# Performance work log

Measured on AMD Instinct MI355X. Metric: run time of the kernel, lower is better.

Reference implementation:

```python
import jax, jax.numpy as jnp
import numpy as np

NUM_NODES = 256
IN_FEAT = 64
HIDDEN = 512
N_CLASSES = 2
BATCH = 256


def setup_inputs() -> dict:
    key = jax.random.key(0)
    ks = jax.random.split(key, 10)
    return {
        "z": jax.random.normal(ks[0], (BATCH, 1, NUM_NODES, NUM_NODES), dtype=jnp.float32),
        "node_emb": jax.random.normal(ks[1], (NUM_NODES, IN_FEAT), dtype=jnp.float32),
        "w1": jax.random.normal(ks[2], (IN_FEAT, HIDDEN), dtype=jnp.float32) * (1.0 / np.sqrt(IN_FEAT)),
        "b1": jnp.zeros((HIDDEN,), dtype=jnp.float32),
        "w2": jax.random.normal(ks[3], (HIDDEN, HIDDEN), dtype=jnp.float32) * (1.0 / np.sqrt(HIDDEN)),
        "b2": jnp.zeros((HIDDEN,), dtype=jnp.float32),
        "w3": jax.random.normal(ks[4], (HIDDEN, HIDDEN), dtype=jnp.float32) * (1.0 / np.sqrt(HIDDEN)),
        "b3": jnp.zeros((HIDDEN,), dtype=jnp.float32),
        "fcw": jax.random.normal(ks[5], (HIDDEN, N_CLASSES), dtype=jnp.float32) * (1.0 / np.sqrt(HIDDEN)),
        "fcb": jnp.zeros((N_CLASSES,), dtype=jnp.float32),
    }


def reference(z, node_emb, w1, b1, w2, b2, w3, b3, fcw, fcb):
    # z: (B, 1, N, N) latent interpreted as weighted adjacency
    z_sq = jnp.squeeze(z, axis=1)                         # (B, N, N)
    A = jax.nn.sigmoid(z_sq)
    A = (A + jnp.swapaxes(A, 1, 2)) * 0.5                  # symmetrize
    A_hat = A + jnp.eye(A.shape[-1], dtype=A.dtype)[None]  # add self loops
    D_hat = jnp.sum(A_hat, axis=2) + 1e-6                  # (B, N) degrees
    d_inv_sqrt = D_hat ** -0.5
    # norm_A = D^{-1/2} A_hat D^{-1/2} via row/col scaling (same math as diag bmm)
    norm_A = A_hat * d_inv_sqrt[:, :, None] * d_inv_sqrt[:, None, :]

    X = jnp.broadcast_to(node_emb[None], (z.shape[0],) + node_emb.shape)  # (B, N, F)
    H1 = jax.nn.relu(jnp.einsum('bij,bjh->bih', norm_A, X @ w1 + b1))
    H2 = jax.nn.relu(jnp.einsum('bij,bjh->bih', norm_A, H1 @ w2 + b2))
    H3 = jax.nn.relu(jnp.einsum('bij,bjh->bih', norm_A, H2 @ w3 + b3))
    graph_emb = jnp.mean(H3, axis=1)                       # (B, H)
    logits = graph_emb @ fcw + fcb                         # (B, n_classes)
    return logits
```

## Files before the change

### kernel.cpp

```cpp
#include <hip/hip_runtime.h>
#include <stdint.h>

#define B_ 256
#define N_ 256
#define F_ 64
#define H_ 512

typedef _Float16 f16;
typedef _Float16 f16x8 __attribute__((ext_vector_type(8)));
typedef _Float16 f16x4 __attribute__((ext_vector_type(4)));
typedef float    f32x4 __attribute__((ext_vector_type(4)));

__device__ __forceinline__ float sigmoidf_(float x) {
    return 1.0f / (1.0f + __expf(-x));
}

__global__ __launch_bounds__(256) void k_sums(const float* __restrict__ z,
                                              f16* __restrict__ S,
                                              float* __restrict__ R,
                                              float* __restrict__ Cpart) {
    int b = blockIdx.y, c = blockIdx.x;
    int tid = threadIdx.x, lane = tid & 63, w = tid >> 6;
    float colacc[4] = {0.f, 0.f, 0.f, 0.f};
    for (int r = 0; r < 16; r++) {
        int i = c * 64 + w * 16 + r;
        size_t base = ((size_t)(b * N_ + i)) * N_;
        float4 v = *(const float4*)(z + base + lane * 4);
        float s0 = sigmoidf_(v.x), s1 = sigmoidf_(v.y),
              s2 = sigmoidf_(v.z), s3 = sigmoidf_(v.w);
        f16x4 sv = { (f16)s0, (f16)s1, (f16)s2, (f16)s3 };
        *(f16x4*)(S + base + lane * 4) = sv;
        colacc[0] += s0; colacc[1] += s1; colacc[2] += s2; colacc[3] += s3;
        float rs = s0 + s1 + s2 + s3;
        for (int off = 32; off; off >>= 1) rs += __shfl_down(rs, off, 64);
        if (lane == 0) R[b * N_ + i] = rs;
    }
    __shared__ float cbuf[4][N_];
    #pragma unroll
    for (int k = 0; k < 4; k++) cbuf[w][lane * 4 + k] = colacc[k];
    __syncthreads();
    float s4 = cbuf[0][tid] + cbuf[1][tid] + cbuf[2][tid] + cbuf[3][tid];
    Cpart[((size_t)c * B_ + b) * N_ + tid] = s4;
}

__global__ __launch_bounds__(256) void k_norma3(const f16* __restrict__ S,
                                                const float* __restrict__ R,
                                                const float* __restrict__ Cpart,
                                                f16* __restrict__ nA) {
    __shared__ f16 T0[128 * 129];
    __shared__ f16 T1[128 * 129];
    __shared__ float Dv[N_];
    int b = blockIdx.y, t = blockIdx.x;
    int tid = threadIdx.x;
    const f16* Sb = S + (size_t)b * N_ * N_;
    f16* Ab = nA + (size_t)b * N_ * N_;

    float cs = Cpart[(size_t)b * N_ + tid]
             + Cpart[((size_t)B_ + b) * N_ + tid]
             + Cpart[((size_t)2 * B_ + b) * N_ + tid]
             + Cpart[((size_t)3 * B_ + b) * N_ + tid];
    Dv[tid] = rsqrtf(1.0f + 1e-6f + 0.5f * (R[b * N_ + tid] + cs));

    auto stage = [&](const f16* src, f16* dst) {
        #pragma unroll
        for (int it = 0; it < 8; it++) {
            int u = it * 256 + tid;
            int r = u >> 4, c8 = (u & 15) * 8;
            *(f16x8*)&dst[r * 129 + c8] = *(const f16x8*)&src[(size_t)r * N_ + c8];
        }
    };
    if (t == 0)      stage(Sb, T0);
    else if (t == 1) stage(Sb + 128 * N_ + 128, T0);
    else           { stage(Sb + 128, T0); stage(Sb + (size_t)128 * N_, T1); }
    __syncthreads();

    auto emit = [&](const f16* Dir, const f16* Mir, int i0, int j0) {
        #pragma unroll
        for (int it = 0; it < 8; it++) {
            int il = it * 16 + (tid >> 4), jl8 = (tid & 15) * 8;
            float di = Dv[i0 + il];
            f16x8 d = *(const f16x8*)&Dir[il * 129 + jl8];
            f16x8 o;
            #pragma unroll
            for (int k = 0; k < 8; k++) {
                float v = 0.5f * ((float)d[k] + (float)Mir[(jl8 + k) * 129 + il]);
                if (i0 + il == j0 + jl8 + k) v += 1.0f;
                o[k] = (f16)(v * di * Dv[j0 + jl8 + k]);
            }
            *(f16x8*)&Ab[(size_t)(i0 + il) * N_ + j0 + jl8] = o;
        }
    };
    if (t == 0)      emit(T0, T0, 0, 0);
    else if (t == 1) emit(T0, T0, 128, 128);
    else           { emit(T0, T1, 0, 128); emit(T1, T0, 128, 0); }
}

__global__ __launch_bounds__(256) void k_prep(const float* __restrict__ ne,
                                              const float* __restrict__ w1,
                                              const float* __restrict__ b1,
                                              const float* __restrict__ w2,
                                              const float* __restrict__ w3,
                                              f16* __restrict__ XW1t,
                                              f16* __restrict__ w2t,
                                              f16* __restrict__ w3t) {
    int bid = blockIdx.x;
    if (bid < 512) {
        int h = bid, node = threadIdx.x;
        float s = b1[h];
        #pragma unroll 8
        for (int k = 0; k < F_; k++) s += ne[node * F_ + k] * w1[k * H_ + h];
        XW1t[h * N_ + node] = (f16)s;
    } else {
        int idx4 = bid - 512;
        int which = idx4 >> 10;
        const float* src = which ? w3 : w2;
        f16* dst = which ? w3t : w2t;
        int idx = (idx4 & 1023) * 256 + threadIdx.x;
        int k = idx >> 9, n = idx & 511;
        dst[n * H_ + k] = (f16)src[k * H_ + n];
    }
}

template <int KDIM, int MODE>
__global__ __launch_bounds__(256, 4) void k_gemm(const f16* __restrict__ A, long aBatch,
                                                 const f16* __restrict__ Bt, long bBatch,
                                                 f16* __restrict__ Out,
                                                 const float* __restrict__ bias,
                                                 float* __restrict__ gp) {
    __shared__ f16 As[128 * 64];
    __shared__ f16 Bs[128 * 64];
    const int tid  = threadIdx.x;
    const int lane = tid & 63, wave = tid >> 6;
    const int wm = wave >> 1, wn = wave & 1;

    const int lin = blockIdx.x;
    const int xcd = lin & 7, q = lin >> 3;
    const int n_t = q & 3, p = q >> 2;
    const int grp = xcd * 64 + p;
    const int b   = grp >> 1, m_t = grp & 1;
    const int m0 = m_t * 128, n0 = n_t * 128;

    const f16* Ab = A + (size_t)b * aBatch;
    const f16* Bb = Bt + (size_t)b * bBatch;

    f32x4 acc[4][4];
    #pragma unroll
    for (int i = 0; i < 4; i++)
        #pragma unroll
        for (int j = 0; j < 4; j++)
            #pragma unroll
            for (int r = 0; r < 4; r++) acc[i][j][r] = 0.0f;

    const int lr = lane >> 3;
    const int kc = (lane & 7) ^ lr;

    const int ln15 = lane & 15;

    for (int kk = 0; kk < KDIM; kk += 64) {
        #pragma unroll
        for (int c = 0; c < 4; c++) {
            int chunk = wave * 4 + c;
            int row = chunk * 8 + lr;
            __builtin_amdgcn_global_load_lds(
                (__attribute__((address_space(1))) void*)(Ab + (size_t)(m0 + row) * KDIM + kk + kc * 8),
                (__attribute__((address_space(3))) void*)(&As[chunk * 512]), 16, 0, 0);
            __builtin_amdgcn_global_load_lds(
                (__attribute__((address_space(1))) void*)(Bb + (size_t)(n0 + row) * KDIM + kk + kc * 8),
                (__attribute__((address_space(3))) void*)(&Bs[chunk * 512]), 16, 0, 0);
        }
        __syncthreads();

        #pragma unroll
        for (int ks = 0; ks < 2; ks++) {
            const int rkc = ks * 4 + (lane >> 4);
            f16x8 aF[4];
            #pragma unroll
            for (int t = 0; t < 4; t++) {
                int ra = wm * 64 + t * 16 + ln15;
                aF[t] = *(const f16x8*)&As[(ra * 8 + (rkc ^ (ra & 7))) * 8];
            }
            #pragma unroll
            for (int h2 = 0; h2 < 2; h2++) {
                f16x8 bF[2];
                #pragma unroll
                for (int t = 0; t < 2; t++) {
                    int rb = wn * 64 + (h2 * 2 + t) * 16 + ln15;
                    bF[t] = *(const f16x8*)&Bs[(rb * 8 + (rkc ^ (rb & 7))) * 8];
                }
                #pragma unroll
                for (int mt = 0; mt < 4; mt++)
                    #pragma unroll
                    for (int t = 0; t < 2; t++)
                        acc[mt][h2 * 2 + t] = __builtin_amdgcn_mfma_f32_16x16x32_f16(aF[mt], bF[t], acc[mt][h2 * 2 + t], 0, 0, 0);
            }
        }
        __syncthreads();
    }

    const int quad = lane >> 4;
    if (MODE == 0) {
        f16* Ob = Out + (size_t)b * (N_ * H_);
        #pragma unroll
        for (int mt = 0; mt < 4; mt++) {
            int node = m0 + wm * 64 + mt * 16 + quad * 4;
            #pragma unroll
            for (int nt = 0; nt < 4; nt++) {
                int h = n0 + wn * 64 + nt * 16 + ln15;
                #pragma unroll
                for (int rr = 0; rr < 4; rr++) {
                    float v = acc[mt][nt][rr];
                    v = v > 0.f ? v : 0.f;
                    Ob[(size_t)(node + rr) * H_ + h] = (f16)v;
                }
            }
        }
    } else if (MODE == 1) {
        f16* Ob = Out + (size_t)b * (H_ * N_);
        #pragma unroll
        for (int nt = 0; nt < 4; nt++) {
            int n = n0 + wn * 64 + nt * 16 + ln15;
            float bv = bias[n];
            #pragma unroll
            for (int mt = 0; mt < 4; mt++) {
                int node = m0 + wm * 64 + mt * 16 + quad * 4;
                f16x4 v;
                #pragma unroll
                for (int rr = 0; rr < 4; rr++) v[rr] = (f16)(acc[mt][nt][rr] + bv);
                *(f16x4*)&Ob[(size_t)n * N_ + node] = v;
            }
        }
    } else {
        float part[4];
        #pragma unroll
        for (int nt = 0; nt < 4; nt++) {
            float partial = 0.f;
            #pragma unroll
            for (int mt = 0; mt < 4; mt++)
                #pragma unroll
                for (int rr = 0; rr < 4; rr++) {
                    float v = acc[mt][nt][rr];
                    partial += (v > 0.f ? v : 0.f);
                }
            partial += __shfl_down(partial, 32, 64);
            partial += __shfl_down(partial, 16, 64);
            part[nt] = partial;
        }
        __syncthreads();
        float* red = (float*)&As[0];
        if (quad == 0) {
            #pragma unroll
            for (int nt = 0; nt < 4; nt++)
                red[wave * 64 + nt * 16 + ln15] = part[nt];
        }
        __syncthreads();
        if (tid < 128) {
            int wnl = tid >> 6, hl = tid & 63;
            float v = red[wnl * 64 + hl] + red[(wnl + 2) * 64 + hl];
            gp[((size_t)m_t * B_ + b) * H_ + n0 + wnl * 64 + hl] = v;
        }
    }
}

__global__ __launch_bounds__(256) void k_logits(const float* __restrict__ gp,
                                                const float* __restrict__ fcw,
                                                const float* __restrict__ fcb,
                                                float* __restrict__ out) {
    int b = blockIdx.x, tid = threadIdx.x;
    const float* g0p = gp + (size_t)b * H_;
    const float* g1p = gp + (size_t)(B_ + b) * H_;
    float g0 = g0p[tid] + g1p[tid];
    float g1 = g0p[tid + 256] + g1p[tid + 256];
    float p0 = g0 * fcw[tid * 2 + 0] + g1 * fcw[(tid + 256) * 2 + 0];
    float p1 = g0 * fcw[tid * 2 + 1] + g1 * fcw[(tid + 256) * 2 + 1];
    for (int off = 32; off; off >>= 1) {
        p0 += __shfl_down(p0, off, 64);
        p1 += __shfl_down(p1, off, 64);
    }
    __shared__ float r0[4], r1[4];
    int lane = tid & 63, w = tid >> 6;
    if (lane == 0) { r0[w] = p0; r1[w] = p1; }
    __syncthreads();
    const float inv = 1.0f / N_;
    if (tid == 0) out[b * 2 + 0] = (r0[0] + r0[1] + r0[2] + r0[3]) * inv + fcb[0];
    if (tid == 1) out[b * 2 + 1] = (r1[0] + r1[1] + r1[2] + r1[3]) * inv + fcb[1];
}

extern "C" void kernel_launch(void* const* d_in, const int* in_sizes, int n_in,
                              void* d_out, int out_size, void* d_ws, size_t ws_size,
                              hipStream_t stream) {
    const float* z   = (const float*)d_in[0];
    const float* ne  = (const float*)d_in[1];
    const float* w1  = (const float*)d_in[2];
    const float* b1  = (const float*)d_in[3];
    const float* w2  = (const float*)d_in[4];
    const float* b2  = (const float*)d_in[5];
    const float* w3  = (const float*)d_in[6];
    const float* b3  = (const float*)d_in[7];
    const float* fcw = (const float*)d_in[8];
    const float* fcb = (const float*)d_in[9];
    float* out = (float*)d_out;

    char* ws = (char*)d_ws;
    f16*   T     = (f16*)(ws + 0);
    float* R     = (float*)(ws + 0);
    float* Cpart = (float*)(ws + 262144);
    f16*   nA    = (f16*)(ws + 67108864);
    f16*   Hh    = (f16*)(ws + 100663296);
    f16*   S     = (f16*)(ws + 100663296);
    float* gpart = (float*)(ws + 100663296);
    f16*   XW1t  = (f16*)(ws + 167772160);
    f16*   w2t   = (f16*)(ws + 168034304);
    f16*   w3t   = (f16*)(ws + 168558592);

    k_sums  <<<dim3(4, B_), 256, 0, stream>>>(z, S, R, Cpart);
    k_norma3<<<dim3(3, B_), 256, 0, stream>>>(S, R, Cpart, nA);
    k_prep  <<<2560,        256, 0, stream>>>(ne, w1, b1, w2, w3, XW1t, w2t, w3t);

    k_gemm<256, 0><<<2048, 256, 0, stream>>>(nA, 65536, XW1t, 0, Hh, nullptr, nullptr);
    k_gemm<512, 1><<<2048, 256, 0, stream>>>(Hh, 131072, w2t, 0, T, b2, nullptr);
    k_gemm<256, 0><<<2048, 256, 0, stream>>>(nA, 65536, T, 131072, Hh, nullptr, nullptr);
    k_gemm<512, 1><<<2048, 256, 0, stream>>>(Hh, 131072, w3t, 0, T, b3, nullptr);
    k_gemm<256, 2><<<2048, 256, 0, stream>>>(nA, 65536, T, 131072, nullptr, nullptr, gpart);

    k_logits<<<B_, 256, 0, stream>>>(gpart, fcw, fcb, out);
}
```

Baseline: 328.0 us.

## Fuse feature transform and adjacency GEMM per layer into one kernel

Layers 2 and 3 previously ran as two GEMM launches each: H@W+b written to global as a transposed intermediate, then norm_A times that intermediate. The new kernel computes a 256-node by 128-hidden tile of H@W+b in registers, stores it to shared memory in a swizzled layout, and immediately multiplies by the adjacency tile for the same batch. This removes the intermediate round trip through global memory and two launches. Each block now covers all 256 nodes, so the final mean reduction is done in-block and writes a single partial per batch instead of two. It uses 512-thread blocks with about 128KB of shared memory and an XCD-aware block mapping, which may limit occupancy.

```diff
diff --git a/kernel.cpp b/kernel.cpp
--- a/kernel.cpp
+++ b/kernel.cpp
@@ -214,39 +214,185 @@
                 }
             }
         }
-    } else if (MODE == 1) {
-        f16* Ob = Out + (size_t)b * (H_ * N_);
-        #pragma unroll
-        for (int nt = 0; nt < 4; nt++) {
-            int n = n0 + wn * 64 + nt * 16 + ln15;
-            float bv = bias[n];
-            #pragma unroll
-            for (int mt = 0; mt < 4; mt++) {
-                int node = m0 + wm * 64 + mt * 16 + quad * 4;
-                f16x4 v;
-                #pragma unroll
-                for (int rr = 0; rr < 4; rr++) v[rr] = (f16)(acc[mt][nt][rr] + bv);
-                *(f16x4*)&Ob[(size_t)n * N_ + node] = v;
+    }
+}
+
+template <int REDUCE>
+__global__ __launch_bounds__(512, 2) void k_fused(const f16* __restrict__ Hin,
+                                                  const f16* __restrict__ Wt,
+                                                  const float* __restrict__ bias,
+                                                  const f16* __restrict__ nA,
+                                                  f16* __restrict__ Hout,
+                                                  float* __restrict__ gp) {
+    __shared__ f16 As[2][16384];
+    __shared__ f16 WU[32768];
+
+    const int tid  = threadIdx.x;
+    const int lane = tid & 63, wave = tid >> 6;
+    const int ln15 = lane & 15, quad = lane >> 4;
+    const int wm = wave >> 1, wn = wave & 1;
+
+    const int lin = blockIdx.x;
+    const int xcd = lin & 7, p = lin >> 3;
+    const int grp = xcd * 128 + p;
+    const int b = grp >> 2, hc = grp & 3;
+
+    const f16* Hb = Hin + (size_t)b * (N_ * H_);
+    const f16* Ab = nA + (size_t)b * (N_ * N_);
+    const f16* Wc = Wt + (size_t)(hc * 128) * H_;
+
+    const int lr = lane >> 3;
+    const int kc = (lane & 7) ^ lr;
+
+    auto stage1 = [&](int buf, int kt) {
+        #pragma unroll
+        for (int c = 0; c < 4; c++) {
+            int chunk = wave * 4 + c;
+            int row = chunk * 8 + lr;
+            __builtin_amdgcn_global_load_lds(
+                (__attribute__((address_space(1))) void*)(Hb + (size_t)row * H_ + kt * 64 + kc * 8),
+                (__attribute__((address_space(3))) void*)(&As[buf][chunk * 512]), 16, 0, 0);
+        }
+        #pragma unroll
+        for (int c = 0; c < 2; c++) {
+            int chunk = wave * 2 + c;
+            int row = chunk * 8 + lr;
+            __builtin_amdgcn_global_load_lds(
+                (__attribute__((address_space(1))) void*)(Wc + (size_t)row * H_ + kt * 64 + kc * 8),
+                (__attribute__((address_space(3))) void*)(&WU[buf * 8192 + chunk * 512]), 16, 0, 0);
+        }
+    };
+    auto stage2 = [&](int buf, int jt) {
+        #pragma unroll
+        for (int c = 0; c < 4; c++) {
+            int chunk = wave * 4 + c;
+            int row = chunk * 8 + lr;
+            __builtin_amdgcn_global_load_lds(
+                (__attribute__((address_space(1))) void*)(Ab + (size_t)row * N_ + jt * 64 + kc * 8),
+                (__attribute__((address_space(3))) void*)(&As[buf][chunk * 512]), 16, 0, 0);
+        }
+    };
+
+    f32x4 acc[4][4];
+    #pragma unroll
+    for (int i = 0; i < 4; i++)
+        #pragma unroll
+        for (int j = 0; j < 4; j++)
+            #pragma unroll
+            for (int r = 0; r < 4; r++) acc[i][j][r] = 0.0f;
+
+    stage1(0, 0);
+    __syncthreads();
+    for (int kt = 0; kt < 8; ++kt) {
+        if (kt < 7) stage1((kt + 1) & 1, kt + 1);
+        else        stage2(0, 0);
+        const int buf = kt & 1;
+        #pragma unroll
+        for (int ks = 0; ks < 2; ks++) {
+            const int rkc = ks * 4 + quad;
+            f16x8 aF[4], bF[4];
+            #pragma unroll
+            for (int t = 0; t < 4; t++) {
+                int ra = wm * 64 + t * 16 + ln15;
+                aF[t] = *(const f16x8*)&As[buf][(ra * 8 + (rkc ^ (ra & 7))) * 8];
+            }
+            #pragma unroll
+            for (int t = 0; t < 4; t++) {
+                int rb = wn * 64 + t * 16 + ln15;
+                bF[t] = *(const f16x8*)&WU[buf * 8192 + (rb * 8 + (rkc ^ (rb & 7))) * 8];
+            }
+            #pragma unroll
+            for (int mt = 0; mt < 4; mt++)
+                #pragma unroll
+                for (int nt = 0; nt < 4; nt++)
+                    acc[mt][nt] = __builtin_amdgcn_mfma_f32_16x16x32_f16(aF[mt], bF[nt], acc[mt][nt], 0, 0, 0);
+        }
+        __syncthreads();
+    }
+
+    #pragma unroll
+    for (int nt = 0; nt < 4; nt++) {
+        int hl = wn * 64 + nt * 16 + ln15;
+        float bv = bias[hc * 128 + hl];
+        #pragma unroll
+        for (int mt = 0; mt < 4; mt++) {
+            int j = wm * 64 + mt * 16 + quad * 4;
+            int slot = (j >> 3) ^ (hl & 7);
+            f16x4 v;
+            #pragma unroll
+            for (int rr = 0; rr < 4; rr++) v[rr] = (f16)(acc[mt][nt][rr] + bv);
+            *(f16x4*)&WU[hl * 256 + slot * 8 + (j & 7)] = v;
+        }
+    }
+    __syncthreads();
+
+    #pragma unroll
+    for (int i = 0; i < 4; i++)
+        #pragma unroll
+        for (int j = 0; j < 4; j++)
+            #pragma unroll
+            for (int r = 0; r < 4; r++) acc[i][j][r] = 0.0f;
+
+    for (int jt = 0; jt < 4; ++jt) {
+        if (jt < 3) stage2((jt + 1) & 1, jt + 1);
+        const int buf = jt & 1;
+        #pragma unroll
+        for (int ks = 0; ks < 2; ks++) {
+            const int rkc = ks * 4 + quad;
+            f16x8 aF[4], bF[4];
+            #pragma unroll
+            for (int t = 0; t < 4; t++) {
+                int ra = wm * 64 + t * 16 + ln15;
+                aF[t] = *(const f16x8*)&As[buf][(ra * 8 + (rkc ^ (ra & 7))) * 8];
+            }
+            #pragma unroll
+            for (int t = 0; t < 4; t++) {
+                int rb = wn * 64 + t * 16 + ln15;
+                int g = jt * 8 + rkc;
+                bF[t] = *(const f16x8*)&WU[rb * 256 + (g ^ (rb & 7)) * 8];
+            }
+            #pragma unroll
+            for (int mt = 0; mt < 4; mt++)
+                #pragma unroll
+                for (int nt = 0; nt < 4; nt++)
+                    acc[mt][nt] = __builtin_amdgcn_mfma_f32_16x16x32_f16(aF[mt], bF[nt], acc[mt][nt], 0, 0, 0);
+        }
+        __syncthreads();
+    }
+
+    if (REDUCE == 0) {
+        f16* Ob = Hout + (size_t)b * (N_ * H_);
+        #pragma unroll
+        for (int mt = 0; mt < 4; mt++) {
+            int node = wm * 64 + mt * 16 + quad * 4;
+            #pragma unroll
+            for (int nt = 0; nt < 4; nt++) {
+                int hg = hc * 128 + wn * 64 + nt * 16 + ln15;
+                #pragma unroll
+                for (int rr = 0; rr < 4; rr++) {
+                    float v = acc[mt][nt][rr];
+                    v = v > 0.f ? v : 0.f;
+                    Ob[(size_t)(node + rr) * H_ + hg] = (f16)v;
+                }
             }
         }
     } else {
         float part[4];
         #pragma unroll
         for (int nt = 0; nt < 4; nt++) {
-            float partial = 0.f;
+            float s = 0.f;
             #pragma unroll
             for (int mt = 0; mt < 4; mt++)
                 #pragma unroll
                 for (int rr = 0; rr < 4; rr++) {
                     float v = acc[mt][nt][rr];
-                    partial += (v > 0.f ? v : 0.f);
+                    s += (v > 0.f ? v : 0.f);
                 }
-            partial += __shfl_down(partial, 32, 64);
-            partial += __shfl_down(partial, 16, 64);
-            part[nt] = partial;
-        }
-        __syncthreads();
-        float* red = (float*)&As[0];
+            s += __shfl_down(s, 32, 64);
+            s += __shfl_down(s, 16, 64);
+            part[nt] = s;
+        }
+        float* red = (float*)&As[0][0];
         if (quad == 0) {
             #pragma unroll
             for (int nt = 0; nt < 4; nt++)
@@ -254,9 +400,10 @@
         }
         __syncthreads();
         if (tid < 128) {
-            int wnl = tid >> 6, hl = tid & 63;
-            float v = red[wnl * 64 + hl] + red[(wnl + 2) * 64 + hl];
-            gp[((size_t)m_t * B_ + b) * H_ + n0 + wnl * 64 + hl] = v;
+            int wnl = tid >> 6, cl = tid & 63;
+            float g = red[(0 * 2 + wnl) * 64 + cl] + red[(1 * 2 + wnl) * 64 + cl]
+                    + red[(2 * 2 + wnl) * 64 + cl] + red[(3 * 2 + wnl) * 64 + cl];
+            gp[(size_t)b * H_ + hc * 128 + tid] = g;
         }
     }
 }
@@ -266,10 +413,9 @@
                                                 const float* __restrict__ fcb,
                                                 float* __restrict__ out) {
     int b = blockIdx.x, tid = threadIdx.x;
-    const float* g0p = gp + (size_t)b * H_;
-    const float* g1p = gp + (size_t)(B_ + b) * H_;
-    float g0 = g0p[tid] + g1p[tid];
-    float g1 = g0p[tid + 256] + g1p[tid + 256];
+    const float* g = gp + (size_t)b * H_;
+    float g0 = g[tid];
+    float g1 = g[tid + 256];
     float p0 = g0 * fcw[tid * 2 + 0] + g1 * fcw[(tid + 256) * 2 + 0];
     float p1 = g0 * fcw[tid * 2 + 1] + g1 * fcw[(tid + 256) * 2 + 1];
     for (int off = 32; off; off >>= 1) {
@@ -317,10 +463,8 @@
     k_prep  <<<2560,        256, 0, stream>>>(ne, w1, b1, w2, w3, XW1t, w2t, w3t);
 
     k_gemm<256, 0><<<2048, 256, 0, stream>>>(nA, 65536, XW1t, 0, Hh, nullptr, nullptr);
-    k_gemm<512, 1><<<2048, 256, 0, stream>>>(Hh, 131072, w2t, 0, T, b2, nullptr);
-    k_gemm<256, 0><<<2048, 256, 0, stream>>>(nA, 65536, T, 131072, Hh, nullptr, nullptr);
-    k_gemm<512, 1><<<2048, 256, 0, stream>>>(Hh, 131072, w3t, 0, T, b3, nullptr);
-    k_gemm<256, 2><<<2048, 256, 0, stream>>>(nA, 65536, T, 131072, nullptr, nullptr, gpart);
+    k_fused<0><<<1024, 512, 0, stream>>>(Hh, w2t, b2, nA, T, nullptr);
+    k_fused<1><<<1024, 512, 0, stream>>>(T, w3t, b3, nA, nullptr, gpart);
 
     k_logits<<<B_, 256, 0, stream>>>(gpart, fcw, fcb, out);
 }
```

New measurement: 320.8 us. 1.02x faster.
